# Kernel tuning notes

Measured on AMD Instinct MI355X. Metric: run time of the kernel, lower is better.

The kernel has to match this reference:

```python
import jax, jax.numpy as jnp
import numpy as np

B, S, D = 2, 2048, 1024
NH, NKV = 16, 4
HD = D // NH
KVD = NKV * HD
NE, MM = 8, 4
INTER = MM * D // NE  # 512
ROPE_BASE = 10000.0
ALPHA, BETA, GATE, DT = 0.95, 0.3, 0.1, 0.1
MU_MIN, MU_MAX, VMAX = 0.5, 1.5, 3.0


def rms_norm(x):
    # torch F.rms_norm with eps=None -> finfo(dtype).eps, no learned weight
    return x * jax.lax.rsqrt(jnp.mean(x * x, axis=-1, keepdims=True) + jnp.finfo(x.dtype).eps)


def rope_tables(seq_len, dtype):
    inv_freq = 1.0 / ROPE_BASE ** (jnp.arange(0, HD, 2, dtype=jnp.float32) / HD)
    t = jnp.arange(seq_len, dtype=jnp.float32)
    freqs = jnp.outer(t, inv_freq)  # [S, HD/2]
    return jnp.cos(freqs).astype(dtype)[None, None], jnp.sin(freqs).astype(dtype)[None, None]


def apply_rotary(x, cos, sin):
    half = x.shape[-1] // 2
    x1, x2 = x[..., :half], x[..., half:]
    return jnp.concatenate((x1 * cos + x2 * sin, -x1 * sin + x2 * cos), axis=-1)


def attention(n, cq_w, ck_w, cv_w, proj_w, q_gain):
    q = jnp.einsum('bsd,od->bso', n, cq_w).reshape(B, S, NH, HD).transpose(0, 2, 1, 3)
    k = jnp.einsum('bsd,od->bso', n, ck_w).reshape(B, S, NKV, HD).transpose(0, 2, 1, 3)
    v = jnp.einsum('bsd,od->bso', n, cv_w).reshape(B, S, NKV, HD).transpose(0, 2, 1, 3)
    q, k = rms_norm(q), rms_norm(k)
    cos, sin = rope_tables(S, q.dtype)
    q, k = apply_rotary(q, cos, sin), apply_rotary(k, cos, sin)
    q = q * q_gain[None, :, None, None]
    rep = NH // NKV  # GQA: repeat kv heads
    k = jnp.repeat(k, rep, axis=1)
    v = jnp.repeat(v, rep, axis=1)
    scale = 1.0 / np.sqrt(HD).astype(np.float32)
    scores = jnp.einsum('bhqd,bhkd->bhqk', q, k) * scale
    causal = jnp.tril(jnp.ones((S, S), bool))
    scores = jnp.where(causal[None, None], scores, jnp.finfo(scores.dtype).min)
    probs = jax.nn.softmax(scores, axis=-1)
    y = jnp.einsum('bhqk,bhkd->bhqd', probs, v)
    y = y.transpose(0, 2, 1, 3).reshape(B, S, D)
    return jnp.einsum('bsd,od->bso', y, proj_w)


def moe(m, gate_up, down, eids):
    # faithful to TokenRoutedMLP: dense per-expert GEMM, masked accumulate
    flat = m.reshape(-1, D)
    fids = eids.reshape(-1)
    out = jnp.zeros_like(flat)
    for e in range(NE):
        gu = flat @ gate_up[e]                       # [T, 2*INTER]
        g, u = gu[:, :INTER], gu[:, INTER:]
        h = (jax.nn.silu(g) * u) @ down[e]           # [T, D]
        out = out + h * (fids == e)[:, None].astype(flat.dtype)
    return out.reshape(B, S, D)


def setup_inputs():
    key = jax.random.key(0)
    ks = jax.random.split(key, 10)
    w = lambda k, shape: jax.random.normal(k, shape, jnp.float32) * 0.02
    return {
        'x': jax.random.normal(ks[0], (B, S, D), jnp.float32),
        'x0': jax.random.normal(ks[1], (B, S, D), jnp.float32),
        'vel': jnp.zeros((B, S, D), jnp.float32),
        'resid_mix': jnp.stack((jnp.ones(D, jnp.float32), jnp.zeros(D, jnp.float32))),
        'attn_scale': jnp.ones(D, jnp.float32),
        'mlp_scale': jnp.ones(D, jnp.float32),
        'cq_w': w(ks[2], (D, D)),
        'ck_w': w(ks[3], (KVD, D)),
        'cv_w': w(ks[4], (KVD, D)),
        'proj_w': w(ks[5], (D, D)),
        'q_gain': jnp.ones(NH, jnp.float32),
        'mu': jnp.full((D,), 1.0, jnp.float32),
        'gate_up': w(ks[6], (NE, D, 2 * INTER)),
        'down': w(ks[7], (NE, INTER, D)),
        'eids': jax.random.randint(ks[8], (B, S), 0, NE),
    }


def reference(x, x0, vel, resid_mix, attn_scale, mlp_scale, cq_w, ck_w, cv_w, proj_w, q_gain, mu, gate_up, down, eids):
    x = resid_mix[0][None, None, :] * x + resid_mix[1][None, None, :] * x0
    n = rms_norm(x)
    x = x + attn_scale[None, None, :] * attention(n, cq_w, ck_w, cv_w, proj_w, q_gain)
    # PID dynamics
    mu_c = jnp.clip(mu, MU_MIN, MU_MAX)
    v_next = jnp.clip(ALPHA * vel - BETA * (x - mu_c[None, None, :]), -VMAX, VMAX)
    x = x + DT * GATE * v_next
    x = x + mlp_scale[None, None, :] * moe(rms_norm(x), gate_up, down, eids)
    return x, v_next
```

## Files before the change

kernel.cpp:

```cpp
#include <hip/hip_runtime.h>
#include <hip/hip_bf16.h>
#include <math.h>

#define NBATCH 2
#define NSEQ   2048
#define NDIM   1024
#define NHEAD  16
#define NKVH   4
#define HDIM   64
#define KVD    256
#define NEXP   8
#define NINTER 512
#define NTOK   (NBATCH*NSEQ)
#define QKVN   1536
#define MAXTILE 40
#define RMS_EPS 1.1920929e-07f
#define LN_10000 9.210340371976184f
#define QSCALE (0.125f * 1.44269504088896f)
#define DEFER_THR 11.5f

typedef __attribute__((ext_vector_type(8))) short bf16x8;
typedef __attribute__((ext_vector_type(4))) short short4v;
typedef __attribute__((ext_vector_type(4))) float f32x4;

__device__ __forceinline__ short f2b(float f) {
  return __builtin_bit_cast(short, (__bf16)f);
}
__device__ __forceinline__ float b2f(short s) {
  unsigned u = ((unsigned)(unsigned short)s) << 16;
  return __builtin_bit_cast(float, u);
}
__device__ __forceinline__ float ex2(float x) {
  float r; asm("v_exp_f32 %0, %1" : "=v"(r) : "v"(x)); return r;
}
__device__ __forceinline__ void load_lds16(const short* g, short* l) {
  __builtin_amdgcn_global_load_lds((const __attribute__((address_space(1))) void*)g,
                                   (__attribute__((address_space(3))) void*)l, 16, 0, 0);
}

__device__ __forceinline__ float wred64(float v) {
#pragma unroll
  for (int m = 32; m >= 1; m >>= 1) v += __shfl_xor(v, m);
  return v;
}

__global__ __launch_bounds__(256) void k_w_cast(
    const float* __restrict__ cq, const float* __restrict__ ck,
    const float* __restrict__ cv, const float* __restrict__ pw,
    short* __restrict__ wqkv, short* __restrict__ wproj) {
  const int row = blockIdx.x;
  const int c = threadIdx.x * 4;
  const float* src; short* dst;
  if (row < 1024)      { src = cq + (size_t)row*NDIM;        dst = wqkv + (size_t)row*NDIM; }
  else if (row < 1280) { src = ck + (size_t)(row-1024)*NDIM; dst = wqkv + (size_t)row*NDIM; }
  else if (row < 1536) { src = cv + (size_t)(row-1280)*NDIM; dst = wqkv + (size_t)row*NDIM; }
  else                 { src = pw + (size_t)(row-1536)*NDIM; dst = wproj + (size_t)(row-1536)*NDIM; }
  float4 v = *(const float4*)(src + c);
  short4v o = {f2b(v.x), f2b(v.y), f2b(v.z), f2b(v.w)};
  *(short4v*)(dst + c) = o;
}

__global__ __launch_bounds__(256) void k_w_transpose(
    const float* __restrict__ in, short* __restrict__ outp, int KIN, int NIN) {
  __shared__ short T[64*66];
  const int kt = blockIdx.x, nt = blockIdx.y, e = blockIdx.z;
  const float* ie = in + (size_t)e*KIN*NIN + (size_t)(kt*64)*NIN + nt*64;
  short* oe = outp + (size_t)e*NIN*KIN + (size_t)(nt*64)*KIN + kt*64;
  const int t = threadIdx.x;
  const int r = t >> 4, c = (t & 15) * 4;
#pragma unroll
  for (int p = 0; p < 4; ++p) {
    float4 v = *(const float4*)(ie + (size_t)(p*16 + r)*NIN + c);
    T[(p*16 + r)*66 + c + 0] = f2b(v.x);
    T[(p*16 + r)*66 + c + 1] = f2b(v.y);
    T[(p*16 + r)*66 + c + 2] = f2b(v.z);
    T[(p*16 + r)*66 + c + 3] = f2b(v.w);
  }
  __syncthreads();
#pragma unroll
  for (int p = 0; p < 4; ++p) {
    int rr = p*16 + r;
    short4v o = {T[(c+0)*66 + rr], T[(c+1)*66 + rr], T[(c+2)*66 + rr], T[(c+3)*66 + rr]};
    *(short4v*)(oe + (size_t)rr*KIN + c) = o;
  }
}

__global__ __launch_bounds__(256) void k_resid_rms(
    const float* __restrict__ x, const float* __restrict__ x0,
    const float* __restrict__ rmix, short* __restrict__ xr, short* __restrict__ nrm) {
  const int row = blockIdx.x;
  const int t = threadIdx.x;
  const int d = t * 4;
  const size_t base = (size_t)row * NDIM + d;
  float4 a  = *(const float4*)(x  + base);
  float4 b  = *(const float4*)(x0 + base);
  float4 m0 = *(const float4*)(rmix + d);
  float4 m1 = *(const float4*)(rmix + NDIM + d);
  float4 r;
  r.x = m0.x*a.x + m1.x*b.x;
  r.y = m0.y*a.y + m1.y*b.y;
  r.z = m0.z*a.z + m1.z*b.z;
  r.w = m0.w*a.w + m1.w*b.w;
  float ss = r.x*r.x + r.y*r.y + r.z*r.z + r.w*r.w;
  ss = wred64(ss);
  __shared__ float wsum[4];
  if ((t & 63) == 0) wsum[t >> 6] = ss;
  __syncthreads();
  float tot = wsum[0] + wsum[1] + wsum[2] + wsum[3];
  float rms = rsqrtf(tot * (1.0f/NDIM) + RMS_EPS);
  short4v xo = {f2b(r.x), f2b(r.y), f2b(r.z), f2b(r.w)};
  short4v no = {f2b(r.x*rms), f2b(r.y*rms), f2b(r.z*rms), f2b(r.w*rms)};
  *(short4v*)(xr + base) = xo;
  *(short4v*)(nrm + base) = no;
}

template <int MODE>
__global__ __launch_bounds__(256) void k_gemm_mfma(
    const short* __restrict__ A, int lda,
    const short* __restrict__ Bw, int K, int N,
    short* __restrict__ Cb, float* __restrict__ Cf, int ldc,
    const int* __restrict__ rowmap, const int* __restrict__ tiletab,
    const int* __restrict__ meta, const float* __restrict__ mscale) {
  __shared__ short sA[128*32];
  __shared__ short sB[128*32];
  int row0, end = 0x7fffffff, e = 0;
  if (MODE == 0) {
    row0 = blockIdx.y * 128;
  } else {
    e = tiletab[2*blockIdx.y];
    if (e < 0) return;
    row0 = tiletab[2*blockIdx.y + 1];
    end = meta[1 + e];
  }
  const int t = threadIdx.x;
  const int w = t >> 6, l = t & 63;
  const int wr = (w >> 1) * 64, wc = (w & 1) * 64;
  const int lrow = l & 15, lk8 = (l >> 4) * 8;
  const int srow0 = w*16 + (l >> 2);
  const int scol = (l & 3) * 8;
  const short* Bp = Bw + (size_t)e * N * K + (size_t)(blockIdx.x * 128) * K;
  const short* gA0;
  const short* gA1;
  if (MODE == 1) {
    int s0 = row0 + srow0;      if (s0 >= NTOK) s0 = NTOK - 1;
    int s1 = row0 + 64 + srow0; if (s1 >= NTOK) s1 = NTOK - 1;
    gA0 = A + (size_t)rowmap[s0] * lda + scol;
    gA1 = A + (size_t)rowmap[s1] * lda + scol;
  } else {
    gA0 = A + (size_t)(row0 + srow0) * lda + scol;
    gA1 = A + (size_t)(row0 + 64 + srow0) * lda + scol;
  }
  const short* gB0 = Bp + (size_t)srow0 * K + scol;
  const short* gB1 = Bp + (size_t)(64 + srow0) * K + scol;
  short* lA0 = sA + (w*16)*32;
  short* lA1 = sA + (64 + w*16)*32;
  short* lB0 = sB + (w*16)*32;
  short* lB1 = sB + (64 + w*16)*32;
  f32x4 acc[4][4];
#pragma unroll
  for (int m = 0; m < 4; ++m)
#pragma unroll
    for (int n = 0; n < 4; ++n) acc[m][n] = 0.f;
  for (int k0 = 0; k0 < K; k0 += 32) {
    __syncthreads();
    load_lds16(gA0, lA0);
    load_lds16(gA1, lA1);
    load_lds16(gB0, lB0);
    load_lds16(gB1, lB1);
    gA0 += 32; gA1 += 32; gB0 += 32; gB1 += 32;
    __syncthreads();
    bf16x8 af[4], bfr[4];
#pragma unroll
    for (int m = 0; m < 4; ++m)
      af[m] = *(const bf16x8*)&sA[(wr + m*16 + lrow)*32 + lk8];
#pragma unroll
    for (int n = 0; n < 4; ++n)
      bfr[n] = *(const bf16x8*)&sB[(wc + n*16 + lrow)*32 + lk8];
#pragma unroll
    for (int m = 0; m < 4; ++m)
#pragma unroll
      for (int n = 0; n < 4; ++n)
        acc[m][n] = __builtin_amdgcn_mfma_f32_16x16x32_bf16(af[m], bfr[n], acc[m][n], 0, 0, 0);
  }
  const int col0 = blockIdx.x * 128;
  if (MODE <= 1) {
#pragma unroll
    for (int m = 0; m < 4; ++m) {
#pragma unroll
      for (int r = 0; r < 4; ++r) {
        int rr = row0 + wr + m*16 + (l >> 4)*4 + r;
        if (rr < end) {
#pragma unroll
          for (int n = 0; n < 4; ++n)
            Cb[(size_t)rr * ldc + col0 + wc + n*16 + lrow] = f2b(acc[m][n][r]);
        }
      }
    }
  } else {
#pragma unroll
    for (int m = 0; m < 4; ++m) {
#pragma unroll
      for (int r = 0; r < 4; ++r) {
        int slot = row0 + wr + m*16 + (l >> 4)*4 + r;
        if (slot < end) {
          int tok = rowmap[slot];
#pragma unroll
          for (int n = 0; n < 4; ++n) {
            int cc = col0 + wc + n*16 + lrow;
            Cf[(size_t)tok * ldc + cc] += mscale[cc] * acc[m][n][r];
          }
        }
      }
    }
  }
}

__global__ __launch_bounds__(256) void k_qk_norm_rope(
    short* __restrict__ qkv, const float* __restrict__ q_gain) {
  const int row = blockIdx.x;
  const int t = threadIdx.x;
  const int w = t >> 6, lane = t & 63;
  const int s = row & (NSEQ - 1);
  const int fi = lane & 31;
  const float fr = (float)s * expf(-(float)fi * (LN_10000 / 32.0f));
  const float co = cosf(fr), si = sinf(fr);
#pragma unroll
  for (int h = w; h < NHEAD; h += 4) {
    short* p = qkv + (size_t)row*QKVN + h*HDIM + lane;
    float v = b2f(*p);
    float ssum = wred64(v*v);
    float rr = rsqrtf(ssum * (1.0f/HDIM) + RMS_EPS);
    float vn = v * rr;
    float partner = __shfl_xor(vn, 32);
    float o = (lane < 32) ? (vn*co + partner*si) : (vn*co - partner*si);
    *p = f2b(o * q_gain[h] * QSCALE);
  }
  if (w < NKVH) {
    short* p = qkv + (size_t)row*QKVN + 1024 + w*HDIM + lane;
    float v = b2f(*p);
    float ssum = wred64(v*v);
    float rr = rsqrtf(ssum * (1.0f/HDIM) + RMS_EPS);
    float vn = v * rr;
    float partner = __shfl_xor(vn, 32);
    float o = (lane < 32) ? (vn*co + partner*si) : (vn*co - partner*si);
    *p = f2b(o);
  }
}

__global__ __launch_bounds__(256) void k_transpose_v(
    const short* __restrict__ qkv, short* __restrict__ vbT) {
  __shared__ short T[64*72];
  const int blk = blockIdx.x;
  const int st = blk & 31, kh = (blk >> 5) & 3, b = blk >> 7;
  const int t = threadIdx.x;
#pragma unroll
  for (int i = 0; i < 2; ++i) {
    int c = t + i*256;
    int s = c >> 3, d0 = (c & 7) * 8;
    bf16x8 v = *(const bf16x8*)(qkv + (size_t)(b*NSEQ + st*64 + s)*QKVN + 1280 + kh*HDIM + d0);
#pragma unroll
    for (int j = 0; j < 8; ++j) T[(d0 + j)*72 + s] = v[j];
  }
  __syncthreads();
#pragma unroll
  for (int i = 0; i < 2; ++i) {
    int c = t + i*256;
    int d = c >> 3, s0 = (c & 7) * 8;
    *(bf16x8*)(vbT + (size_t)((b*NKVH + kh)*HDIM + d)*NSEQ + st*64 + s0) = *(bf16x8*)&T[d*72 + s0];
  }
}

__global__ __launch_bounds__(256) void k_attn_mfma(
    const short* __restrict__ qkv, const short* __restrict__ vbT, short* __restrict__ y) {
  __shared__ short Ks[2][64*72];
  __shared__ short Vt[2][64*72];
  __shared__ short Ps[64*72];
  const int t = threadIdx.x;
  const int l = t & 63, w = t >> 6;
  const int lrow = l & 15, g = l >> 4, lk8 = g * 8;
  const int bid = blockIdx.x;
  int qt = bid & 15;
  const int h = (bid >> 4) & 15, b = bid >> 8;
  if (b & 1) qt = 15 - qt;
  const int kh = h >> 2;
  bf16x8 qf[2][2];
#pragma unroll
  for (int qra = 0; qra < 2; ++qra) {
    int qrow_g = b*NSEQ + qt*128 + qra*64 + w*16 + lrow;
#pragma unroll
    for (int hf = 0; hf < 2; ++hf)
      qf[qra][hf] = *(const bf16x8*)(qkv + (size_t)qrow_g*QKVN + h*HDIM + hf*32 + lk8);
  }
  const int r0a = t >> 3;
  const int d0a = (t & 7) * 8;
  const short* kgbase = qkv + 1024 + (size_t)kh*HDIM;
  const short* vgbase = vbT + (size_t)((b*NKVH + kh)*HDIM)*NSEQ;
  bf16x8 kr0, kr1, vr0, vr1;
#define LOADKV(KT) do { \
    kr0 = *(const bf16x8*)(kgbase + (size_t)(b*NSEQ + (KT)*64 + r0a)*QKVN + d0a); \
    kr1 = *(const bf16x8*)(kgbase + (size_t)(b*NSEQ + (KT)*64 + r0a + 32)*QKVN + d0a); \
    vr0 = *(const bf16x8*)(vgbase + (size_t)r0a*NSEQ + (KT)*64 + d0a); \
    vr1 = *(const bf16x8*)(vgbase + (size_t)(r0a + 32)*NSEQ + (KT)*64 + d0a); \
  } while (0)
  float m_i[2] = {-INFINITY, -INFINITY};
  float l_i[2] = {0.f, 0.f};
  f32x4 O[2][4];
#pragma unroll
  for (int qra = 0; qra < 2; ++qra)
#pragma unroll
    for (int db = 0; db < 4; ++db) O[qra][db] = 0.f;
  const int ktmax = 2*qt + 1;
  LOADKV(0);
  for (int kt = 0; kt <= ktmax; ++kt) {
    const int buf = kt & 1;
    *(bf16x8*)&Ks[buf][r0a*72 + d0a] = kr0;
    *(bf16x8*)&Ks[buf][(r0a + 32)*72 + d0a] = kr1;
    *(bf16x8*)&Vt[buf][r0a*72 + d0a] = vr0;
    *(bf16x8*)&Vt[buf][(r0a + 32)*72 + d0a] = vr1;
    __syncthreads();
    if (kt < ktmax) LOADKV(kt + 1);
    const int qra0 = (kt == ktmax) ? 1 : 0;
    bf16x8 pf[2][2];
#pragma unroll
    for (int qra = 0; qra < 2; ++qra) {
      if (qra >= qra0) {
        f32x4 sc[4];
#pragma unroll
        for (int nb = 0; nb < 4; ++nb) sc[nb] = 0.f;
        __builtin_amdgcn_s_setprio(1);
#pragma unroll
        for (int nb = 0; nb < 4; ++nb) {
          bf16x8 kf0 = *(const bf16x8*)&Ks[buf][(nb*16 + lrow)*72 + lk8];
          bf16x8 kf1 = *(const bf16x8*)&Ks[buf][(nb*16 + lrow)*72 + 32 + lk8];
          sc[nb] = __builtin_amdgcn_mfma_f32_16x16x32_bf16(kf0, qf[qra][0], sc[nb], 0, 0, 0);
          sc[nb] = __builtin_amdgcn_mfma_f32_16x16x32_bf16(kf1, qf[qra][1], sc[nb], 0, 0, 0);
        }
        __builtin_amdgcn_s_setprio(0);
        if (kt >= 2*qt) {
          int qg = qt*128 + qra*64 + w*16 + lrow;
#pragma unroll
          for (int nb = 0; nb < 4; ++nb)
#pragma unroll
            for (int r = 0; r < 4; ++r)
              if (kt*64 + nb*16 + g*4 + r > qg) sc[nb][r] = -INFINITY;
        }
        float rm = sc[0][0];
#pragma unroll
        for (int nb = 0; nb < 4; ++nb)
#pragma unroll
          for (int r = 0; r < 4; ++r) rm = fmaxf(rm, sc[nb][r]);
        rm = fmaxf(rm, __shfl_xor(rm, 16));
        rm = fmaxf(rm, __shfl_xor(rm, 32));
        if (!__all(rm <= m_i[qra] + DEFER_THR)) {
          float mn = fmaxf(m_i[qra], rm);
          float fac = ex2(m_i[qra] - mn);
          l_i[qra] *= fac;
          m_i[qra] = mn;
#pragma unroll
          for (int r = 0; r < 4; ++r) {
            float ff = __shfl(fac, g*4 + r);
#pragma unroll
            for (int db = 0; db < 4; ++db) O[qra][db][r] *= ff;
          }
        }
        float rs = 0.f;
#pragma unroll
        for (int nb = 0; nb < 4; ++nb) {
#pragma unroll
          for (int r = 0; r < 4; ++r) {
            float p = ex2(sc[nb][r] - m_i[qra]);
            sc[nb][r] = p;
            rs += p;
          }
        }
        rs += __shfl_xor(rs, 16);
        rs += __shfl_xor(rs, 32);
        l_i[qra] += rs;
        short* prow = &Ps[(w*16 + lrow)*72];
#pragma unroll
        for (int nb = 0; nb < 4; ++nb) {
          short4v pk = {f2b(sc[nb][0]), f2b(sc[nb][1]), f2b(sc[nb][2]), f2b(sc[nb][3])};
          *(short4v*)(prow + nb*16 + g*4) = pk;
        }
        pf[qra][0] = *(const bf16x8*)&Ps[(w*16 + lrow)*72 + lk8];
        pf[qra][1] = *(const bf16x8*)&Ps[(w*16 + lrow)*72 + 32 + lk8];
      }
    }
    __builtin_amdgcn_s_setprio(1);
#pragma unroll
    for (int db = 0; db < 4; ++db) {
      bf16x8 vf0 = *(const bf16x8*)&Vt[buf][(db*16 + lrow)*72 + lk8];
      bf16x8 vf1 = *(const bf16x8*)&Vt[buf][(db*16 + lrow)*72 + 32 + lk8];
      if (qra0 == 0) {
        O[0][db] = __builtin_amdgcn_mfma_f32_16x16x32_bf16(pf[0][0], vf0, O[0][db], 0, 0, 0);
        O[0][db] = __builtin_amdgcn_mfma_f32_16x16x32_bf16(pf[0][1], vf1, O[0][db], 0, 0, 0);
      }
      O[1][db] = __builtin_amdgcn_mfma_f32_16x16x32_bf16(pf[1][0], vf0, O[1][db], 0, 0, 0);
      O[1][db] = __builtin_amdgcn_mfma_f32_16x16x32_bf16(pf[1][1], vf1, O[1][db], 0, 0, 0);
    }
    __builtin_amdgcn_s_setprio(0);
  }
#undef LOADKV
#pragma unroll
  for (int qra = 0; qra < 2; ++qra) {
    float linv = 1.0f / l_i[qra];
#pragma unroll
    for (int r = 0; r < 4; ++r) {
      float inv = __shfl(linv, g*4 + r);
      int rowo = b*NSEQ + qt*128 + qra*64 + w*16 + g*4 + r;
#pragma unroll
      for (int db = 0; db < 4; ++db)
        y[(size_t)rowo*NDIM + h*HDIM + db*16 + lrow] = f2b(O[qra][db][r] * inv);
    }
  }
}

__global__ __launch_bounds__(256) void k_fuse_vel(
    const short* __restrict__ xr, const short* __restrict__ aout,
    const float* __restrict__ vel, const float* __restrict__ ascale,
    const float* __restrict__ mu, float* __restrict__ out, short* __restrict__ mbuf) {
  const int row = blockIdx.x;
  const int t = threadIdx.x;
  const int d = t * 4;
  const size_t base = (size_t)row * NDIM + d;
  short4v a4 = *(const short4v*)(xr + base);
  short4v o4 = *(const short4v*)(aout + base);
  float4 vv = *(const float4*)(vel + base);
  float4 as = *(const float4*)(ascale + d);
  float4 mu4 = *(const float4*)(mu + d);
  float xs[4], vns[4];
  const float asl[4] = {as.x, as.y, as.z, as.w};
  const float mul[4] = {mu4.x, mu4.y, mu4.z, mu4.w};
  const float vvl[4] = {vv.x, vv.y, vv.z, vv.w};
#pragma unroll
  for (int i = 0; i < 4; ++i) {
    float x1 = b2f(a4[i]) + asl[i] * b2f(o4[i]);
    float muc = fminf(fmaxf(mul[i], 0.5f), 1.5f);
    float vn = fminf(fmaxf(0.95f*vvl[i] - 0.3f*(x1 - muc), -3.f), 3.f);
    xs[i] = x1 + 0.01f*vn;
    vns[i] = vn;
  }
  float4 x2 = {xs[0], xs[1], xs[2], xs[3]};
  float4 vnq = {vns[0], vns[1], vns[2], vns[3]};
  *(float4*)(out + base) = x2;
  *(float4*)(out + (size_t)NTOK*NDIM + base) = vnq;
  float ss = xs[0]*xs[0] + xs[1]*xs[1] + xs[2]*xs[2] + xs[3]*xs[3];
  ss = wred64(ss);
  __shared__ float wsum[4];
  if ((t & 63) == 0) wsum[t >> 6] = ss;
  __syncthreads();
  float tot = wsum[0] + wsum[1] + wsum[2] + wsum[3];
  float rms = rsqrtf(tot * (1.0f/NDIM) + RMS_EPS);
  short4v m4 = {f2b(xs[0]*rms), f2b(xs[1]*rms), f2b(xs[2]*rms), f2b(xs[3]*rms)};
  *(short4v*)(mbuf + base) = m4;
}

__global__ __launch_bounds__(256) void k_route(
    const int* __restrict__ eids, int* __restrict__ rowmap,
    int* __restrict__ tiletab, int* __restrict__ meta) {
  __shared__ int cnt[NEXP];
  __shared__ int ctr[NEXP];
  const int t = threadIdx.x;
  if (t < NEXP) cnt[t] = 0;
  __syncthreads();
  for (int i = t; i < NTOK; i += 256) atomicAdd(&cnt[eids[i]], 1);
  __syncthreads();
  if (t == 0) {
    int off = 0, tile = 0;
    for (int e = 0; e < NEXP; ++e) {
      ctr[e] = off;
      int nt_e = (cnt[e] + 127) >> 7;
      for (int j = 0; j < nt_e; ++j) { tiletab[2*tile] = e; tiletab[2*tile+1] = off + j*128; ++tile; }
      off += cnt[e];
      meta[1 + e] = off;
    }
    meta[0] = tile;
    for (int j = tile; j < MAXTILE; ++j) { tiletab[2*j] = -1; tiletab[2*j+1] = 0; }
  }
  __syncthreads();
  for (int i = t; i < NTOK; i += 256) {
    int e = eids[i];
    int slot = atomicAdd(&ctr[e], 1);
    rowmap[slot] = i;
  }
}

__global__ __launch_bounds__(256) void k_silu(
    const short* __restrict__ gu, short* __restrict__ hb) {
  int gid = blockIdx.x * 256 + threadIdx.x;
  int row = gid >> 7, c4 = (gid & 127) * 4;
  short4v g = *(const short4v*)(gu + (size_t)row*1024 + c4);
  short4v u = *(const short4v*)(gu + (size_t)row*1024 + 512 + c4);
  short4v o;
#pragma unroll
  for (int i = 0; i < 4; ++i) {
    float gf = b2f(g[i]), uf = b2f(u[i]);
    o[i] = f2b(gf / (1.0f + __expf(-gf)) * uf);
  }
  *(short4v*)(hb + (size_t)row*512 + c4) = o;
}

extern "C" void kernel_launch(void* const* d_in, const int* in_sizes, int n_in,
                              void* d_out, int out_size, void* d_ws, size_t ws_size,
                              hipStream_t stream) {
  const float* x      = (const float*)d_in[0];
  const float* x0     = (const float*)d_in[1];
  const float* vel    = (const float*)d_in[2];
  const float* rmix   = (const float*)d_in[3];
  const float* ascale = (const float*)d_in[4];
  const float* mscale = (const float*)d_in[5];
  const float* cq_w   = (const float*)d_in[6];
  const float* ck_w   = (const float*)d_in[7];
  const float* cv_w   = (const float*)d_in[8];
  const float* proj_w = (const float*)d_in[9];
  const float* q_gain = (const float*)d_in[10];
  const float* mu     = (const float*)d_in[11];
  const float* gate_up= (const float*)d_in[12];
  const float* down   = (const float*)d_in[13];
  const int*   eids   = (const int*)d_in[14];
  float* out = (float*)d_out;
  char* base = (char*)d_ws;

  const size_t MB = 1024*1024;
  short* wqkv  = (short*)base;
  short* wproj = (short*)(base + 3*MB);
  int*   rowmap  = (int*)(base + 5*MB);
  int*   tiletab = rowmap + NTOK;
  int*   meta    = tiletab + 2*MAXTILE;
  short* wgu_t = (short*)(base + 6*MB);
  short* hbuf  = wgu_t;
  short* xr    = (short*)(base + 22*MB);
  short* gu    = xr;
  short* nbuf  = (short*)(base + 30*MB);
  short* ybuf  = nbuf;
  short* mbuf  = nbuf;
  short* wdn_t = nbuf;
  short* qkv   = (short*)(base + 38*MB);
  short* aout  = qkv;
  short* vbT   = (short*)(base + 50*MB);

  k_w_cast<<<2560, 256, 0, stream>>>(cq_w, ck_w, cv_w, proj_w, wqkv, wproj);
  k_w_transpose<<<dim3(16, 16, 8), 256, 0, stream>>>(gate_up, wgu_t, 1024, 1024);
  k_resid_rms<<<NTOK, 256, 0, stream>>>(x, x0, rmix, xr, nbuf);
  k_gemm_mfma<0><<<dim3(QKVN/128, NTOK/128), 256, 0, stream>>>(
      nbuf, NDIM, wqkv, NDIM, QKVN, qkv, nullptr, QKVN, nullptr, nullptr, nullptr, nullptr);
  k_qk_norm_rope<<<NTOK, 256, 0, stream>>>(qkv, q_gain);
  k_transpose_v<<<NBATCH*NKVH*(NSEQ/64), 256, 0, stream>>>(qkv, vbT);
  k_attn_mfma<<<NBATCH*NHEAD*(NSEQ/128), 256, 0, stream>>>(qkv, vbT, ybuf);
  k_gemm_mfma<0><<<dim3(NDIM/128, NTOK/128), 256, 0, stream>>>(
      ybuf, NDIM, wproj, NDIM, NDIM, aout, nullptr, NDIM, nullptr, nullptr, nullptr, nullptr);
  k_fuse_vel<<<NTOK, 256, 0, stream>>>(xr, aout, vel, ascale, mu, out, mbuf);
  k_route<<<1, 256, 0, stream>>>(eids, rowmap, tiletab, meta);
  k_gemm_mfma<1><<<dim3(1024/128, MAXTILE), 256, 0, stream>>>(
      mbuf, NDIM, wgu_t, NDIM, 1024, gu, nullptr, 1024, rowmap, tiletab, meta, nullptr);
  k_w_transpose<<<dim3(8, 16, 8), 256, 0, stream>>>(down, wdn_t, 512, 1024);
  k_silu<<<(NTOK*512)/(4*256), 256, 0, stream>>>(gu, hbuf);
  k_gemm_mfma<2><<<dim3(NDIM/128, MAXTILE), 256, 0, stream>>>(
      hbuf, NINTER, wdn_t, NINTER, NDIM, nullptr, out, NDIM, rowmap, tiletab, meta, mscale);
}
```

Measured before the change: 236.5 us.

## Split long causal attention query tiles across two blocks with a combine kernel

Long query tiles (qt 8..15) are split into two key ranges handled by separate blocks. Each block writes unnormalized fp32 partial outputs plus running max and sum, and a new combine kernel merges them with a log-sum-exp rescale. Short tiles still run in one pass. This balances the causal workload across 768 blocks instead of 512 to cut tail imbalance, at the cost of extra fp32 partial traffic and one more launch. The gate_up weight transpose is moved after attention because its workspace is now reused for the partials.

```diff
diff --git a/kernel.cpp b/kernel.cpp
--- a/kernel.cpp
+++ b/kernel.cpp
@@ -18,6 +18,7 @@
 #define LN_10000 9.210340371976184f
 #define QSCALE (0.125f * 1.44269504088896f)
 #define DEFER_THR 11.5f
+#define LOG2E 1.44269504088896f
 
 typedef __attribute__((ext_vector_type(8))) short bf16x8;
 typedef __attribute__((ext_vector_type(4))) short short4v;
@@ -271,7 +272,8 @@
 }
 
 __global__ __launch_bounds__(256) void k_attn_mfma(
-    const short* __restrict__ qkv, const short* __restrict__ vbT, short* __restrict__ y) {
+    const short* __restrict__ qkv, const short* __restrict__ vbT,
+    short* __restrict__ y, float* __restrict__ Opart, float* __restrict__ ml) {
   __shared__ short Ks[2][64*72];
   __shared__ short Vt[2][64*72];
   __shared__ short Ps[64*72];
@@ -279,9 +281,24 @@
   const int l = t & 63, w = t >> 6;
   const int lrow = l & 15, g = l >> 4, lk8 = g * 8;
   const int bid = blockIdx.x;
-  int qt = bid & 15;
-  const int h = (bid >> 4) & 15, b = bid >> 8;
-  if (b & 1) qt = 15 - qt;
+  int qt, bh, kt0, kt1;
+  bool split;
+  if (bid < 512) {
+    split = true;
+    const int item = bid >> 1, part = bid & 1;
+    qt = 15 - (item >> 5);
+    bh = item & 31;
+    kt0 = part ? (qt + 1) : 0;
+    kt1 = part ? (2*qt + 2) : (qt + 1);
+  } else {
+    split = false;
+    const int u = bid - 512;
+    qt = 7 - (u >> 5);
+    bh = u & 31;
+    kt0 = 0;
+    kt1 = 2*qt + 2;
+  }
+  const int b = bh >> 4, h = bh & 15;
   const int kh = h >> 2;
   bf16x8 qf[2][2];
 #pragma unroll
@@ -309,17 +326,16 @@
   for (int qra = 0; qra < 2; ++qra)
 #pragma unroll
     for (int db = 0; db < 4; ++db) O[qra][db] = 0.f;
-  const int ktmax = 2*qt + 1;
-  LOADKV(0);
-  for (int kt = 0; kt <= ktmax; ++kt) {
+  LOADKV(kt0);
+  for (int kt = kt0; kt < kt1; ++kt) {
     const int buf = kt & 1;
     *(bf16x8*)&Ks[buf][r0a*72 + d0a] = kr0;
     *(bf16x8*)&Ks[buf][(r0a + 32)*72 + d0a] = kr1;
     *(bf16x8*)&Vt[buf][r0a*72 + d0a] = vr0;
     *(bf16x8*)&Vt[buf][(r0a + 32)*72 + d0a] = vr1;
     __syncthreads();
-    if (kt < ktmax) LOADKV(kt + 1);
-    const int qra0 = (kt == ktmax) ? 1 : 0;
+    if (kt + 1 < kt1) LOADKV(kt + 1);
+    const int qra0 = (kt == 2*qt + 1) ? 1 : 0;
     bf16x8 pf[2][2];
 #pragma unroll
     for (int qra = 0; qra < 2; ++qra) {
@@ -401,17 +417,65 @@
     __builtin_amdgcn_s_setprio(0);
   }
 #undef LOADKV
-#pragma unroll
-  for (int qra = 0; qra < 2; ++qra) {
-    float linv = 1.0f / l_i[qra];
-#pragma unroll
-    for (int r = 0; r < 4; ++r) {
-      float inv = __shfl(linv, g*4 + r);
-      int rowo = b*NSEQ + qt*128 + qra*64 + w*16 + g*4 + r;
-#pragma unroll
-      for (int db = 0; db < 4; ++db)
-        y[(size_t)rowo*NDIM + h*HDIM + db*16 + lrow] = f2b(O[qra][db][r] * inv);
+  if (!split) {
+#pragma unroll
+    for (int qra = 0; qra < 2; ++qra) {
+      float linv = 1.0f / l_i[qra];
+#pragma unroll
+      for (int r = 0; r < 4; ++r) {
+        float inv = __shfl(linv, g*4 + r);
+        int rowo = b*NSEQ + qt*128 + qra*64 + w*16 + g*4 + r;
+#pragma unroll
+        for (int db = 0; db < 4; ++db)
+          y[(size_t)rowo*NDIM + h*HDIM + db*16 + lrow] = f2b(O[qra][db][r] * inv);
+      }
     }
+  } else {
+    float* Op = Opart + (size_t)bid * 128 * 64;
+#pragma unroll
+    for (int qra = 0; qra < 2; ++qra) {
+#pragma unroll
+      for (int r = 0; r < 4; ++r) {
+        int row = qra*64 + w*16 + g*4 + r;
+#pragma unroll
+        for (int db = 0; db < 4; ++db)
+          Op[(size_t)row*64 + db*16 + lrow] = O[qra][db][r];
+      }
+      if (g == 0) {
+        int row = qra*64 + w*16 + lrow;
+        ml[(size_t)bid*256 + row*2 + 0] = m_i[qra];
+        ml[(size_t)bid*256 + row*2 + 1] = l_i[qra];
+      }
+    }
+  }
+}
+
+__global__ __launch_bounds__(256) void k_attn_combine(
+    const float* __restrict__ Opart, const float* __restrict__ ml, short* __restrict__ y) {
+  const int item = blockIdx.x;
+  const int qt = 15 - (item >> 5);
+  const int bh = item & 31;
+  const int b = bh >> 4, h = bh & 15;
+  const int t = threadIdx.x;
+  const int row = t >> 1, dh = (t & 1) * 32;
+  const float* O1 = Opart + (size_t)(item*2 + 0) * 8192;
+  const float* O2 = Opart + (size_t)(item*2 + 1) * 8192;
+  const float* ml1 = ml + (size_t)(item*2 + 0) * 256;
+  const float* ml2 = ml + (size_t)(item*2 + 1) * 256;
+  float m1 = ml1[row*2], l1 = ml1[row*2 + 1];
+  float m2 = ml2[row*2], l2 = ml2[row*2 + 1];
+  float M = fmaxf(m1, m2);
+  float w1 = ex2(m1 - M), w2 = ex2(m2 - M);
+  float inv = 1.0f / (l1*w1 + l2*w2);
+  const int rowo = b*NSEQ + qt*128 + row;
+  short* yp = y + (size_t)rowo*NDIM + h*HDIM + dh;
+#pragma unroll
+  for (int d = 0; d < 32; d += 4) {
+    float4 o1 = *(const float4*)(O1 + (size_t)row*64 + dh + d);
+    float4 o2 = *(const float4*)(O2 + (size_t)row*64 + dh + d);
+    short4v o = {f2b((o1.x*w1 + o2.x*w2)*inv), f2b((o1.y*w1 + o2.y*w2)*inv),
+                 f2b((o1.z*w1 + o2.z*w2)*inv), f2b((o1.w*w1 + o2.w*w2)*inv)};
+    *(short4v*)(yp + d) = o;
   }
 }
 
@@ -523,10 +587,12 @@
 
   const size_t MB = 1024*1024;
   short* wqkv  = (short*)base;
+  float* ml    = (float*)base;
   short* wproj = (short*)(base + 3*MB);
   int*   rowmap  = (int*)(base + 5*MB);
   int*   tiletab = rowmap + NTOK;
   int*   meta    = tiletab + 2*MAXTILE;
+  float* Opart = (float*)(base + 6*MB);
   short* wgu_t = (short*)(base + 6*MB);
   short* hbuf  = wgu_t;
   short* xr    = (short*)(base + 22*MB);
@@ -540,13 +606,14 @@
   short* vbT   = (short*)(base + 50*MB);
 
   k_w_cast<<<2560, 256, 0, stream>>>(cq_w, ck_w, cv_w, proj_w, wqkv, wproj);
-  k_w_transpose<<<dim3(16, 16, 8), 256, 0, stream>>>(gate_up, wgu_t, 1024, 1024);
   k_resid_rms<<<NTOK, 256, 0, stream>>>(x, x0, rmix, xr, nbuf);
   k_gemm_mfma<0><<<dim3(QKVN/128, NTOK/128), 256, 0, stream>>>(
       nbuf, NDIM, wqkv, NDIM, QKVN, qkv, nullptr, QKVN, nullptr, nullptr, nullptr, nullptr);
   k_qk_norm_rope<<<NTOK, 256, 0, stream>>>(qkv, q_gain);
   k_transpose_v<<<NBATCH*NKVH*(NSEQ/64), 256, 0, stream>>>(qkv, vbT);
-  k_attn_mfma<<<NBATCH*NHEAD*(NSEQ/128), 256, 0, stream>>>(qkv, vbT, ybuf);
+  k_attn_mfma<<<768, 256, 0, stream>>>(qkv, vbT, ybuf, Opart, ml);
+  k_attn_combine<<<256, 256, 0, stream>>>(Opart, ml, ybuf);
+  k_w_transpose<<<dim3(16, 16, 8), 256, 0, stream>>>(gate_up, wgu_t, 1024, 1024);
   k_gemm_mfma<0><<<dim3(NDIM/128, NTOK/128), 256, 0, stream>>>(
       ybuf, NDIM, wproj, NDIM, NDIM, aout, nullptr, NDIM, nullptr, nullptr, nullptr, nullptr);
   k_fuse_vel<<<NTOK, 256, 0, stream>>>(xr, aout, vel, ascale, mu, out, mbuf);
```

Result: slower. 246.5 us (+4.2%).
